# Optimization experiments

Measured on AMD Instinct MI355X. Metric: run time of the kernel, lower is better.

Reference implementation:

```python
import jax, jax.numpy as jnp
import numpy as np
import math

EPS = 1e-6


def setup_inputs() -> dict:
    key = jax.random.key(0)
    k1, k2 = jax.random.split(key)
    B, S, D, F = 4, 4096, 2048, 2048
    x = jax.random.normal(k1, (B, S, D), dtype=jnp.float32)
    weight = jax.random.normal(k2, (F, D), dtype=jnp.float32) / np.sqrt(D)
    alpha = jnp.ones((1,), dtype=jnp.float32)
    bias = jnp.zeros((F,), dtype=jnp.float32)
    return {"x": x, "weight": weight, "alpha": alpha, "bias": bias}


def reference(x, weight, alpha, bias):
    F = weight.shape[0]
    # y: [B, S, F]
    y = jnp.einsum("bsd,fd->bsf", x, weight)
    x_sq = jnp.sum(x * x, axis=-1, keepdims=True)        # [B, S, 1]
    w_sq = jnp.sum(weight * weight, axis=-1)              # [F]
    distances = x_sq + w_sq - 2.0 * y                     # squared Euclidean dist
    out = (y * y) / (distances + EPS)
    scale = (math.sqrt(F) / math.log(1.0 + F)) ** alpha   # alpha shape (1,) broadcasts
    out = out * scale + bias
    return out
```

## Files before the change

### kernel.cpp

```cpp
#include <hip/hip_runtime.h>
#include <hip/hip_bf16.h>
#include <cstdint>
#include <cstddef>


typedef __bf16 bf16_t;
typedef __bf16 bf16x8 __attribute__((ext_vector_type(8)));
typedef __bf16 bf16x4 __attribute__((ext_vector_type(4)));
typedef float f32x4 __attribute__((ext_vector_type(4)));

constexpr int M_DIM = 16384;
constexpr int N_DIM = 2048;
constexpr int K_DIM = 2048;
constexpr int BM = 256, BN = 256, BK = 64;
constexpr int KT = K_DIM / BK;
constexpr int SEG = 128 * 64;

__device__ __forceinline__ void async16(const bf16_t* g, bf16_t* l) {
    __builtin_amdgcn_global_load_lds(
        (const __attribute__((address_space(1))) void*)g,
        (__attribute__((address_space(3))) void*)l,
        16, 0, 0);
}

__global__ __launch_bounds__(256) void prep_convert(const float* __restrict__ x,
                                                    const float* __restrict__ w,
                                                    bf16_t* __restrict__ xb,
                                                    bf16_t* __restrict__ wb,
                                                    float* __restrict__ xsq,
                                                    float* __restrict__ wsq) {
    const int lane = threadIdx.x & 63;
    const int wv = threadIdx.x >> 6;
    const int base = blockIdx.x * 8 + wv * 2;
#pragma unroll
    for (int it = 0; it < 2; ++it) {
        const int row = base + it;
        const float* src;
        bf16_t* dstb;
        float* dsts;
        if (row < M_DIM) {
            src = x + (size_t)row * K_DIM;
            dstb = xb + (size_t)row * K_DIM;
            dsts = xsq + row;
        } else {
            const int r = row - M_DIM;
            src = w + (size_t)r * K_DIM;
            dstb = wb + (size_t)r * K_DIM;
            dsts = wsq + r;
        }
        const float4* s4 = (const float4*)src;
        bf16x4* d4 = (bf16x4*)dstb;
        float s = 0.0f;
#pragma unroll
        for (int j = 0; j < 8; ++j) {
            const float4 a = s4[lane + j * 64];
            s += a.x * a.x + a.y * a.y + a.z * a.z + a.w * a.w;
            bf16x4 v = { (bf16_t)a.x, (bf16_t)a.y, (bf16_t)a.z, (bf16_t)a.w };
            d4[lane + j * 64] = v;
        }
#pragma unroll
        for (int off = 32; off > 0; off >>= 1) s += __shfl_down(s, off, 64);
        if (lane == 0) *dsts = s;
    }
}

__global__ __launch_bounds__(512, 2) void yat_gemm(const bf16_t* __restrict__ A,
                                                   const bf16_t* __restrict__ Bw,
                                                   const float* __restrict__ xsq,
                                                   const float* __restrict__ wsq,
                                                   const float* __restrict__ bias,
                                                   const float* __restrict__ alpha,
                                                   float* __restrict__ out) {
    __shared__ bf16_t sA[4 * SEG];
    __shared__ bf16_t sB[4 * SEG];

    const int tid = (int)threadIdx.x;
    const int lane = tid & 63;
    const int wv = tid >> 6;
    const int wm = wv >> 2;
    const int wn = wv & 3;

    const int bm = (int)blockIdx.x >> 3;
    const int bn = (int)blockIdx.x & 7;

    const int frm = lane & 15;
    const int jch = lane >> 4;
    const int sx = frm & 7;

    const int st_r = tid >> 3;
    const int st_g = (tid & 7) ^ (st_r & 7);
    const bf16_t* Ast = A + (size_t)(bm * BM + st_r) * K_DIM + st_g * 8;
    const bf16_t* Bst = Bw + (size_t)(bn * BN + st_r) * K_DIM + st_g * 8;

    auto stageA2 = [&](int kt) {
        if (kt >= KT) return;
#pragma unroll
        for (int h = 0; h < 2; ++h) {
            bf16_t* d = sA + ((kt * 2 + h) & 3) * SEG + tid * 8;
            const bf16_t* s = Ast + (size_t)(h * 128) * K_DIM + kt * 64;
            async16(s, d);
            async16(s + (size_t)64 * K_DIM, d + 4096);
        }
    };
    auto stageB1 = [&](int kt, int h) {
        if (kt >= KT) return;
        bf16_t* d = sB + ((kt * 2 + h) & 3) * SEG + tid * 8;
        const bf16_t* s = Bst + (size_t)(h * 128) * K_DIM + kt * 64;
        async16(s, d);
        async16(s + (size_t)64 * K_DIM, d + 4096);
    };

    f32x4 acc[8][4] = {};
    bf16x8 afA[2][2], afB[2][2];
    bf16x8 bfrA[4][2], bfrB[4][2];

#define AF_READ(DST, KTN, QN)                                                  \
    {                                                                          \
        const int aslot_ = (((KTN) * 2 + wm) & 3) * SEG;                       \
        _Pragma("unroll") for (int i2 = 0; i2 < 2; ++i2)                       \
            _Pragma("unroll") for (int kk = 0; kk < 2; ++kk)                   \
                DST[i2][kk] = *(const bf16x8*)&sA[aslot_ +                     \
                    (((QN) * 2 + i2) * 16 + frm) * 64 + (((kk * 4 + jch) ^ sx) * 8)]; \
    }
#define BF_READ(DST, BJ0, KTB)                                                 \
    {                                                                          \
        const int bslot_ = (((KTB) * 2 + (wn >> 1)) & 3) * SEG;                \
        _Pragma("unroll") for (int jj = 0; jj < 2; ++jj)                       \
            _Pragma("unroll") for (int kk = 0; kk < 2; ++kk)                   \
                DST[(BJ0) + jj][kk] = *(const bf16x8*)&sB[bslot_ +             \
                    ((wn & 1) * 64 + ((BJ0) + jj) * 16 + frm) * 64 +           \
                    (((kk * 4 + jch) ^ sx) * 8)];                              \
    }
#define MFMA16(QC, AFC, BFC)                                                   \
    __builtin_amdgcn_s_setprio(1);                                             \
    _Pragma("unroll") for (int kk = 0; kk < 2; ++kk)                           \
        _Pragma("unroll") for (int i2 = 0; i2 < 2; ++i2)                       \
            _Pragma("unroll") for (int j = 0; j < 4; ++j)                      \
                acc[(QC) * 2 + i2][j] = __builtin_amdgcn_mfma_f32_16x16x32_bf16( \
                    AFC[i2][kk], BFC[j][kk], acc[(QC) * 2 + i2][j], 0, 0, 0);  \
    __builtin_amdgcn_s_setprio(0);
#define SCHED0 __builtin_amdgcn_sched_barrier(0);
#define SBAR asm volatile("s_barrier" ::: "memory");
#define VMC4 asm volatile("s_waitcnt vmcnt(4)" ::: "memory");
#define VMC(SKT)                                                               \
    if ((SKT) < KT) { VMC4 } else { asm volatile("s_waitcnt vmcnt(0)" ::: "memory"); }

    stageA2(0);
    stageB1(0, 0); stageB1(0, 1);
    stageB1(1, 0); stageB1(1, 1);
    VMC4
    SBAR
    AF_READ(afA, 0, 0)
    BF_READ(bfrA, 0, 0)
    BF_READ(bfrA, 2, 0)

#pragma unroll 1
    for (int u = 0; u < KT / 2; ++u) {
        const int a = 2 * u, b = a + 1;
        AF_READ(afB, a, 1)
        stageA2(b);
        SCHED0
        MFMA16(0, afA, bfrA)
        VMC4
        SBAR
        AF_READ(afA, a, 2)
        BF_READ(bfrB, 0, b)
        stageB1(a + 2, 0);
        SCHED0
        MFMA16(1, afB, bfrA)
        SBAR
        AF_READ(afB, a, 3)
        BF_READ(bfrB, 2, b)
        stageB1(a + 2, 1);
        SCHED0
        MFMA16(2, afA, bfrA)
        VMC(a + 2)
        SBAR
        AF_READ(afA, b, 0)
        SCHED0
        MFMA16(3, afB, bfrA)
        SBAR
        AF_READ(afB, b, 1)
        stageA2(a + 2);
        SCHED0
        MFMA16(0, afA, bfrB)
        VMC(a + 2)
        SBAR
        AF_READ(afA, b, 2)
        BF_READ(bfrA, 0, a + 2)
        stageB1(b + 2, 0);
        SCHED0
        MFMA16(1, afB, bfrB)
        SBAR
        AF_READ(afB, b, 3)
        BF_READ(bfrA, 2, a + 2)
        stageB1(b + 2, 1);
        SCHED0
        MFMA16(2, afA, bfrB)
        VMC(b + 2)
        SBAR
        AF_READ(afA, a + 2, 0)
        SCHED0
        MFMA16(3, afB, bfrB)
        SBAR
    }
#undef AF_READ
#undef BF_READ
#undef MFMA16
#undef SCHED0
#undef SBAR
#undef VMC4
#undef VMC

    const float sc = powf(sqrtf((float)N_DIM) / logf(1.0f + (float)N_DIM), alpha[0]);
    float wsq_c[4], bias_c[4];
#pragma unroll
    for (int j = 0; j < 4; ++j) {
        const int col = bn * BN + wn * 64 + j * 16 + frm;
        wsq_c[j] = wsq[col];
        bias_c[j] = bias[col];
    }
#pragma unroll
    for (int i = 0; i < 8; ++i) {
#pragma unroll
        for (int r = 0; r < 4; ++r) {
            const int row = bm * BM + wm * 128 + i * 16 + jch * 4 + r;
            const float xs = xsq[row];
            float* orow = out + (size_t)row * N_DIM + bn * BN + wn * 64 + frm;
#pragma unroll
            for (int j = 0; j < 4; ++j) {
                const float y = acc[i][j][r];
                const float d = xs + wsq_c[j] - 2.0f * y + 1e-6f;
                orow[j * 16] = (y * y) / d * sc + bias_c[j];
            }
        }
    }
}

extern "C" void kernel_launch(void* const* d_in, const int* in_sizes, int n_in,
                              void* d_out, int out_size, void* d_ws, size_t ws_size,
                              hipStream_t stream) {
    (void)in_sizes; (void)n_in; (void)out_size; (void)ws_size;
    const float* x = (const float*)d_in[0];
    const float* w = (const float*)d_in[1];
    const float* alpha = (const float*)d_in[2];
    const float* bias = (const float*)d_in[3];
    float* out = (float*)d_out;

    bf16_t* xb = (bf16_t*)d_ws;
    bf16_t* wb = xb + (size_t)M_DIM * K_DIM;
    float* xsq = (float*)(wb + (size_t)N_DIM * K_DIM);
    float* wsq = xsq + M_DIM;

    prep_convert<<<(M_DIM + N_DIM) / 8, 256, 0, stream>>>(x, w, xb, wb, xsq, wsq);
    yat_gemm<<<(M_DIM / BM) * (N_DIM / BN), 512, 0, stream>>>(xb, wb, xsq, wsq, bias, alpha, out);
}
```

Baseline: 363.7 us.

## Process two M-tiles per block with precomputed LDS pointers and peeled k-loop

Each workgroup now computes two consecutive 256-row output tiles for the same N-tile, halving the grid from 512 to 256 blocks. LDS read and write addresses are precomputed as pointer bases, so slot indices no longer need runtime arithmetic, and the final k-iteration pair is peeled so the loop body needs no bounds checks or conditional waitcnt. The aim is to cut per-iteration address overhead and to let the second tile's epilogue and prologue overlap with other blocks. The trade-off is a grid of 256 blocks, which may underfill a 256-CU device at 2 blocks/CU, and each block has a serialized epilogue and prologue between its two tiles.

```diff
diff --git a/kernel.cpp b/kernel.cpp
--- a/kernel.cpp
+++ b/kernel.cpp
@@ -80,8 +80,9 @@
     const int wm = wv >> 2;
     const int wn = wv & 3;
 
-    const int bm = (int)blockIdx.x >> 3;
     const int bn = (int)blockIdx.x & 7;
+    const int q = (int)blockIdx.x >> 3;
+    const int bm0 = q * 2, bm1 = q * 2 + 1;
 
     const int frm = lane & 15;
     const int jch = lane >> 4;
@@ -89,48 +90,40 @@
 
     const int st_r = tid >> 3;
     const int st_g = (tid & 7) ^ (st_r & 7);
-    const bf16_t* Ast = A + (size_t)(bm * BM + st_r) * K_DIM + st_g * 8;
     const bf16_t* Bst = Bw + (size_t)(bn * BN + st_r) * K_DIM + st_g * 8;
-
-    auto stageA2 = [&](int kt) {
-        if (kt >= KT) return;
-#pragma unroll
-        for (int h = 0; h < 2; ++h) {
-            bf16_t* d = sA + ((kt * 2 + h) & 3) * SEG + tid * 8;
-            const bf16_t* s = Ast + (size_t)(h * 128) * K_DIM + kt * 64;
-            async16(s, d);
-            async16(s + (size_t)64 * K_DIM, d + 4096);
-        }
-    };
-    auto stageB1 = [&](int kt, int h) {
-        if (kt >= KT) return;
-        bf16_t* d = sB + ((kt * 2 + h) & 3) * SEG + tid * 8;
-        const bf16_t* s = Bst + (size_t)(h * 128) * K_DIM + kt * 64;
-        async16(s, d);
-        async16(s + (size_t)64 * K_DIM, d + 4096);
-    };
+    const bf16_t* Ast = A + (size_t)(bm0 * BM + st_r) * K_DIM + st_g * 8;
+
+    bf16_t* aSD[4];
+    bf16_t* bSD[4];
+#pragma unroll
+    for (int s = 0; s < 4; ++s) {
+        aSD[s] = sA + s * SEG + tid * 8;
+        bSD[s] = sB + s * SEG + tid * 8;
+    }
+
+    const bf16_t* aRB[2][2];
+    const bf16_t* bRB[2][2];
+#pragma unroll
+    for (int p = 0; p < 2; ++p)
+#pragma unroll
+        for (int kk = 0; kk < 2; ++kk) {
+            aRB[p][kk] = sA + (wm + 2 * p) * SEG + frm * BK + ((kk * 4 + jch) ^ sx) * 8;
+            bRB[p][kk] = sB + ((wn >> 1) + 2 * p) * SEG + ((wn & 1) * 64 + frm) * BK
+                         + ((kk * 4 + jch) ^ sx) * 8;
+        }
 
     f32x4 acc[8][4] = {};
     bf16x8 afA[2][2], afB[2][2];
     bf16x8 bfrA[4][2], bfrB[4][2];
 
-#define AF_READ(DST, KTN, QN)                                                  \
-    {                                                                          \
-        const int aslot_ = (((KTN) * 2 + wm) & 3) * SEG;                       \
-        _Pragma("unroll") for (int i2 = 0; i2 < 2; ++i2)                       \
-            _Pragma("unroll") for (int kk = 0; kk < 2; ++kk)                   \
-                DST[i2][kk] = *(const bf16x8*)&sA[aslot_ +                     \
-                    (((QN) * 2 + i2) * 16 + frm) * 64 + (((kk * 4 + jch) ^ sx) * 8)]; \
-    }
-#define BF_READ(DST, BJ0, KTB)                                                 \
-    {                                                                          \
-        const int bslot_ = (((KTB) * 2 + (wn >> 1)) & 3) * SEG;                \
-        _Pragma("unroll") for (int jj = 0; jj < 2; ++jj)                       \
-            _Pragma("unroll") for (int kk = 0; kk < 2; ++kk)                   \
-                DST[(BJ0) + jj][kk] = *(const bf16x8*)&sB[bslot_ +             \
-                    ((wn & 1) * 64 + ((BJ0) + jj) * 16 + frm) * 64 +           \
-                    (((kk * 4 + jch) ^ sx) * 8)];                              \
-    }
+#define AF_READ(DST, PAR, QN)                                                  \
+    _Pragma("unroll") for (int i2 = 0; i2 < 2; ++i2)                           \
+        _Pragma("unroll") for (int kk = 0; kk < 2; ++kk)                       \
+            DST[i2][kk] = *(const bf16x8*)(aRB[PAR][kk] + ((QN) * 2 + i2) * 1024);
+#define BF_READ(DST, BJ0, PAR)                                                 \
+    _Pragma("unroll") for (int jj = 0; jj < 2; ++jj)                           \
+        _Pragma("unroll") for (int kk = 0; kk < 2; ++kk)                       \
+            DST[(BJ0) + jj][kk] = *(const bf16x8*)(bRB[PAR][kk] + ((BJ0) + jj) * 1024);
 #define MFMA16(QC, AFC, BFC)                                                   \
     __builtin_amdgcn_s_setprio(1);                                             \
     _Pragma("unroll") for (int kk = 0; kk < 2; ++kk)                           \
@@ -141,100 +134,115 @@
     __builtin_amdgcn_s_setprio(0);
 #define SCHED0 __builtin_amdgcn_sched_barrier(0);
 #define SBAR asm volatile("s_barrier" ::: "memory");
-#define VMC4 asm volatile("s_waitcnt vmcnt(4)" ::: "memory");
-#define VMC(SKT)                                                               \
-    if ((SKT) < KT) { VMC4 } else { asm volatile("s_waitcnt vmcnt(0)" ::: "memory"); }
-
-    stageA2(0);
-    stageB1(0, 0); stageB1(0, 1);
-    stageB1(1, 0); stageB1(1, 1);
-    VMC4
+#define VM4 asm volatile("s_waitcnt vmcnt(4)" ::: "memory");
+#define VM0 asm volatile("s_waitcnt vmcnt(0)" ::: "memory");
+#define STAGE_A(kt, S0, S1)                                                    \
+    {                                                                          \
+        const bf16_t* s_ = Ast + (size_t)(kt) * 64;                            \
+        async16(s_, aSD[S0]);                                                  \
+        async16(s_ + (size_t)64 * K_DIM, aSD[S0] + 4096);                      \
+        async16(s_ + (size_t)128 * K_DIM, aSD[S1]);                            \
+        async16(s_ + (size_t)192 * K_DIM, aSD[S1] + 4096);                     \
+    }
+#define STAGE_B(kt, S0, S1)                                                    \
+    {                                                                          \
+        const bf16_t* s_ = Bst + (size_t)(kt) * 64;                            \
+        async16(s_, bSD[S0]);                                                  \
+        async16(s_ + (size_t)64 * K_DIM, bSD[S0] + 4096);                      \
+        async16(s_ + (size_t)128 * K_DIM, bSD[S1]);                            \
+        async16(s_ + (size_t)192 * K_DIM, bSD[S1] + 4096);                     \
+    }
+
+    auto stagepro = [&]() {
+        STAGE_A(0, 0, 1)
+        STAGE_B(0, 0, 1)
+        STAGE_B(1, 2, 3)
+    };
+    auto preloop = [&]() {
+        AF_READ(afA, 0, 0)
+        BF_READ(bfrA, 0, 0)
+        BF_READ(bfrA, 2, 0)
+    };
+
+    auto kloop = [&]() {
+#pragma unroll 1
+        for (int u = 0; u < KT / 2 - 1; ++u) {
+            const int tb = 2 * u + 1, t2 = 2 * u + 2, t3 = 2 * u + 3;
+            AF_READ(afB, 0, 1) STAGE_A(tb, 2, 3) SCHED0 MFMA16(0, afA, bfrA) VM4 SBAR
+            AF_READ(afA, 0, 2) BF_READ(bfrB, 0, 1) STAGE_B(t2, 0, 1) SCHED0 MFMA16(1, afB, bfrA) SBAR
+            AF_READ(afB, 0, 3) BF_READ(bfrB, 2, 1) SCHED0 MFMA16(2, afA, bfrA) VM4 SBAR
+            AF_READ(afA, 1, 0) SCHED0 MFMA16(3, afB, bfrA) SBAR
+            AF_READ(afB, 1, 1) STAGE_A(t2, 0, 1) SCHED0 MFMA16(0, afA, bfrB) VM4 SBAR
+            AF_READ(afA, 1, 2) BF_READ(bfrA, 0, 0) STAGE_B(t3, 2, 3) SCHED0 MFMA16(1, afB, bfrB) SBAR
+            AF_READ(afB, 1, 3) BF_READ(bfrA, 2, 0) SCHED0 MFMA16(2, afA, bfrB) VM4 SBAR
+            AF_READ(afA, 0, 0) SCHED0 MFMA16(3, afB, bfrB) SBAR
+        }
+        AF_READ(afB, 0, 1) STAGE_A(KT - 1, 2, 3) SCHED0 MFMA16(0, afA, bfrA) VM4 SBAR
+        AF_READ(afA, 0, 2) BF_READ(bfrB, 0, 1) SCHED0 MFMA16(1, afB, bfrA) SBAR
+        AF_READ(afB, 0, 3) BF_READ(bfrB, 2, 1) SCHED0 MFMA16(2, afA, bfrA) VM0 SBAR
+        AF_READ(afA, 1, 0) SCHED0 MFMA16(3, afB, bfrA) SBAR
+        AF_READ(afB, 1, 1) SCHED0 MFMA16(0, afA, bfrB) SBAR
+        AF_READ(afA, 1, 2) SCHED0 MFMA16(1, afB, bfrB) SBAR
+        AF_READ(afB, 1, 3) SCHED0 MFMA16(2, afA, bfrB) SBAR
+        SCHED0 MFMA16(3, afB, bfrB) SBAR
+    };
+
+    auto epilogue = [&](int bmv) {
+        const float sc = powf(sqrtf((float)N_DIM) / logf(1.0f + (float)N_DIM), alpha[0]);
+        float wsq_c[4], bias_c[4];
+#pragma unroll
+        for (int j = 0; j < 4; ++j) {
+            const int col = bn * BN + wn * 64 + j * 16 + frm;
+            wsq_c[j] = wsq[col];
+            bias_c[j] = bias[col];
+        }
+#pragma unroll
+        for (int i = 0; i < 8; ++i) {
+#pragma unroll
+            for (int r = 0; r < 4; ++r) {
+                const int row = bmv * BM + wm * 128 + i * 16 + jch * 4 + r;
+                const float xs = xsq[row];
+                float* orow = out + (size_t)row * N_DIM + bn * BN + wn * 64 + frm;
+#pragma unroll
+                for (int j = 0; j < 4; ++j) {
+                    const float y = acc[i][j][r];
+                    const float d = xs + wsq_c[j] - 2.0f * y + 1e-6f;
+                    orow[j * 16] = (y * y) / d * sc + bias_c[j];
+                }
+            }
+        }
+    };
+
+    stagepro();
+    VM4 SBAR
+    preloop();
+    kloop();
+    epilogue(bm0);
+
     SBAR
-    AF_READ(afA, 0, 0)
-    BF_READ(bfrA, 0, 0)
-    BF_READ(bfrA, 2, 0)
-
-#pragma unroll 1
-    for (int u = 0; u < KT / 2; ++u) {
-        const int a = 2 * u, b = a + 1;
-        AF_READ(afB, a, 1)
-        stageA2(b);
-        SCHED0
-        MFMA16(0, afA, bfrA)
-        VMC4
-        SBAR
-        AF_READ(afA, a, 2)
-        BF_READ(bfrB, 0, b)
-        stageB1(a + 2, 0);
-        SCHED0
-        MFMA16(1, afB, bfrA)
-        SBAR
-        AF_READ(afB, a, 3)
-        BF_READ(bfrB, 2, b)
-        stageB1(a + 2, 1);
-        SCHED0
-        MFMA16(2, afA, bfrA)
-        VMC(a + 2)
-        SBAR
-        AF_READ(afA, b, 0)
-        SCHED0
-        MFMA16(3, afB, bfrA)
-        SBAR
-        AF_READ(afB, b, 1)
-        stageA2(a + 2);
-        SCHED0
-        MFMA16(0, afA, bfrB)
-        VMC(a + 2)
-        SBAR
-        AF_READ(afA, b, 2)
-        BF_READ(bfrA, 0, a + 2)
-        stageB1(b + 2, 0);
-        SCHED0
-        MFMA16(1, afB, bfrB)
-        SBAR
-        AF_READ(afB, b, 3)
-        BF_READ(bfrA, 2, a + 2)
-        stageB1(b + 2, 1);
-        SCHED0
-        MFMA16(2, afA, bfrB)
-        VMC(b + 2)
-        SBAR
-        AF_READ(afA, a + 2, 0)
-        SCHED0
-        MFMA16(3, afB, bfrB)
-        SBAR
-    }
+    Ast = A + (size_t)(bm1 * BM + st_r) * K_DIM + st_g * 8;
+    stagepro();
+    VM4 SBAR
+    preloop();
+#pragma unroll
+    for (int i = 0; i < 8; ++i)
+#pragma unroll
+        for (int j = 0; j < 4; ++j) {
+            const f32x4 z = {};
+            acc[i][j] = z;
+        }
+    kloop();
+    epilogue(bm1);
+
 #undef AF_READ
 #undef BF_READ
 #undef MFMA16
 #undef SCHED0
 #undef SBAR
-#undef VMC4
-#undef VMC
-
-    const float sc = powf(sqrtf((float)N_DIM) / logf(1.0f + (float)N_DIM), alpha[0]);
-    float wsq_c[4], bias_c[4];
-#pragma unroll
-    for (int j = 0; j < 4; ++j) {
-        const int col = bn * BN + wn * 64 + j * 16 + frm;
-        wsq_c[j] = wsq[col];
-        bias_c[j] = bias[col];
-    }
-#pragma unroll
-    for (int i = 0; i < 8; ++i) {
-#pragma unroll
-        for (int r = 0; r < 4; ++r) {
-            const int row = bm * BM + wm * 128 + i * 16 + jch * 4 + r;
-            const float xs = xsq[row];
-            float* orow = out + (size_t)row * N_DIM + bn * BN + wn * 64 + frm;
-#pragma unroll
-            for (int j = 0; j < 4; ++j) {
-                const float y = acc[i][j][r];
-                const float d = xs + wsq_c[j] - 2.0f * y + 1e-6f;
-                orow[j * 16] = (y * y) / d * sc + bias_c[j];
-            }
-        }
-    }
+#undef VM4
+#undef VM0
+#undef STAGE_A
+#undef STAGE_B
 }
 
 extern "C" void kernel_launch(void* const* d_in, const int* in_sizes, int n_in,
@@ -253,5 +261,5 @@
     float* wsq = xsq + M_DIM;
 
     prep_convert<<<(M_DIM + N_DIM) / 8, 256, 0, stream>>>(x, w, xb, wb, xsq, wsq);
-    yat_gemm<<<(M_DIM / BM) * (N_DIM / BN), 512, 0, stream>>>(xb, wb, xsq, wsq, bias, alpha, out);
-}
+    yat_gemm<<<(M_DIM / BM) * (N_DIM / BN) / 2, 512, 0, stream>>>(xb, wb, xsq, wsq, bias, alpha, out);
+}
```

Measured after the change: 404.0 us. +11.1%, slower.
